# Performance work log

Hardware: AMD Instinct MI355X
Metric: run time of the kernel (lower is better)

## Reference

```python
import jax, jax.numpy as jnp
import numpy as np

D_MODEL = 512
N_HEADS = 4  # d_model >= 8 -> 4 heads
HEAD_DIM = D_MODEL // N_HEADS
D_FF = 4 * D_MODEL


def setup_inputs() -> dict:
    key = jax.random.key(0)
    ks = jax.random.split(key, 8)
    B, T = 4, 2048
    s = 0.02
    return {
        "x": jax.random.normal(ks[0], (B, T, D_MODEL), dtype=jnp.float32),
        "ln1_g": jnp.ones((D_MODEL,), jnp.float32),
        "ln1_b": jnp.zeros((D_MODEL,), jnp.float32),
        "w_qkv": jax.random.normal(ks[1], (D_MODEL, 3 * D_MODEL), jnp.float32) * s,
        "w_proj": jax.random.normal(ks[2], (D_MODEL, D_MODEL), jnp.float32) * s,
        "ln2_g": jnp.ones((D_MODEL,), jnp.float32),
        "ln2_b": jnp.zeros((D_MODEL,), jnp.float32),
        "w_ff1": jax.random.normal(ks[3], (D_MODEL, D_FF), jnp.float32) * s,
        "w_ff2": jax.random.normal(ks[4], (D_FF, D_MODEL), jnp.float32) * s,
    }


def _layernorm(x, g, b, eps=1e-5):
    mu = jnp.mean(x, axis=-1, keepdims=True)
    var = jnp.var(x, axis=-1, keepdims=True)
    return (x - mu) * jax.lax.rsqrt(var + eps) * g + b


def _attention(x, w_qkv, w_proj):
    B, T, C = x.shape
    qkv = x @ w_qkv  # [B,T,3C]
    q, k, v = jnp.split(qkv, 3, axis=-1)
    # [B,H,T,Dh]
    q = q.reshape(B, T, N_HEADS, HEAD_DIM).transpose(0, 2, 1, 3)
    k = k.reshape(B, T, N_HEADS, HEAD_DIM).transpose(0, 2, 1, 3)
    v = v.reshape(B, T, N_HEADS, HEAD_DIM).transpose(0, 2, 1, 3)
    scale = 1.0 / jnp.sqrt(jnp.asarray(HEAD_DIM, x.dtype))
    scores = jnp.einsum("bhqd,bhkd->bhqk", q, k) * scale
    causal = jnp.tril(jnp.ones((T, T), bool))
    scores = jnp.where(causal, scores, -jnp.inf)
    attn = jax.nn.softmax(scores, axis=-1)
    out = jnp.einsum("bhqk,bhkd->bhqd", attn, v)
    out = out.transpose(0, 2, 1, 3).reshape(B, T, C)
    return out @ w_proj


def reference(x, ln1_g, ln1_b, w_qkv, w_proj, ln2_g, ln2_b, w_ff1, w_ff2):
    x = x + _attention(_layernorm(x, ln1_g, ln1_b), w_qkv, w_proj)
    h = _layernorm(x, ln2_g, ln2_b)
    h = jax.nn.gelu(h @ w_ff1, approximate=False) @ w_ff2
    return x + h
```

## Files before the change

kernel.cpp:

```cpp
#include <hip/hip_runtime.h>
#include <cstdint>

typedef unsigned short u16;
typedef __attribute__((ext_vector_type(8))) short short8;
typedef __attribute__((ext_vector_type(4))) float floatx4;

#define BT    8192
#define TSEQ  2048
#define NBAT  4
#define CMOD  512
#define NH    4
#define HD    128
#define DFF   2048
#define CQKV  1536

__device__ __forceinline__ u16 f2bf(float f) {
  union { float f; uint32_t u; } v; v.f = f;
  uint32_t r = v.u + 0x7FFFu + ((v.u >> 16) & 1u);
  return (u16)(r >> 16);
}

__device__ __forceinline__ float exp2a(float x) {
  float r; asm("v_exp_f32 %0, %1" : "=v"(r) : "v"(x)); return r;
}
__device__ __forceinline__ float rcpa(float x) {
  float r; asm("v_rcp_f32 %0, %1" : "=v"(r) : "v"(x)); return r;
}

typedef __attribute__((address_space(1))) const unsigned int ga_u32;
typedef __attribute__((address_space(3))) unsigned int ls_u32;
__device__ __forceinline__ void glds16(const u16* g, u16* l) {
  __builtin_amdgcn_global_load_lds((ga_u32*)g, (ls_u32*)l, 16, 0, 0);
}

__global__ __launch_bounds__(256) void transpose_cast(const float* __restrict__ W,
                                                      u16* __restrict__ Wt, int K, int N) {
  __shared__ float tile[32][33];
  int n0 = blockIdx.x * 32, k0 = blockIdx.y * 32;
  int tx = threadIdx.x & 31, ty = threadIdx.x >> 5;
  #pragma unroll
  for (int r = 0; r < 32; r += 8)
    tile[r + ty][tx] = W[(size_t)(k0 + r + ty) * N + n0 + tx];
  __syncthreads();
  #pragma unroll
  for (int r = 0; r < 32; r += 8)
    Wt[(size_t)(n0 + r + ty) * K + k0 + tx] = f2bf(tile[tx][r + ty]);
}

__global__ __launch_bounds__(256) void ln_kernel(const float* __restrict__ x,
                                                 const float* __restrict__ g,
                                                 const float* __restrict__ b,
                                                 u16* __restrict__ out) {
  int row = blockIdx.x * 4 + (threadIdx.x >> 6);
  int lane = threadIdx.x & 63;
  const float4* xr = (const float4*)(x + (size_t)row * CMOD);
  float4 a = xr[lane], c = xr[lane + 64];
  float s = a.x + a.y + a.z + a.w + c.x + c.y + c.z + c.w;
  float q = a.x*a.x + a.y*a.y + a.z*a.z + a.w*a.w
          + c.x*c.x + c.y*c.y + c.z*c.z + c.w*c.w;
  #pragma unroll
  for (int o = 32; o; o >>= 1) { s += __shfl_xor(s, o); q += __shfl_xor(q, o); }
  float mu = s * (1.0f / CMOD);
  float rstd = rsqrtf(q * (1.0f / CMOD) - mu * mu + 1e-5f);
  const float4* gr = (const float4*)g;
  const float4* br = (const float4*)b;
  float4 g0 = gr[lane], g1 = gr[lane + 64], b0 = br[lane], b1 = br[lane + 64];
  u16* orow = out + (size_t)row * CMOD;
  int i0 = lane * 4, i1 = (lane + 64) * 4;
  orow[i0 + 0] = f2bf((a.x - mu) * rstd * g0.x + b0.x);
  orow[i0 + 1] = f2bf((a.y - mu) * rstd * g0.y + b0.y);
  orow[i0 + 2] = f2bf((a.z - mu) * rstd * g0.z + b0.z);
  orow[i0 + 3] = f2bf((a.w - mu) * rstd * g0.w + b0.w);
  orow[i1 + 0] = f2bf((c.x - mu) * rstd * g1.x + b1.x);
  orow[i1 + 1] = f2bf((c.y - mu) * rstd * g1.y + b1.y);
  orow[i1 + 2] = f2bf((c.z - mu) * rstd * g1.z + b1.z);
  orow[i1 + 3] = f2bf((c.w - mu) * rstd * g1.w + b1.w);
}

template <int EPI>
__global__ __launch_bounds__(256) void gemm_kernel(
    const u16* __restrict__ A, const u16* __restrict__ Bt, int K,
    const float* __restrict__ resid, float* __restrict__ outf,
    u16* __restrict__ ob0, u16* __restrict__ ob1, u16* __restrict__ ob2) {
  constexpr int LDT = 40;
  __shared__ __align__(16) u16 As[128 * LDT];
  __shared__ __align__(16) u16 Bs[128 * LDT];
  int tid = threadIdx.x;
  int lane = tid & 63, wave = tid >> 6;
  int lane16 = lane & 15, quad = lane >> 4;
  int m0 = blockIdx.y * 128, n0 = blockIdx.x * 128;
  int wm = (wave >> 1) * 64, wn = (wave & 1) * 64;
  int srow = tid >> 2, skc = (tid & 3) * 8;

  floatx4 acc[4][4];
  #pragma unroll
  for (int i = 0; i < 4; i++)
    #pragma unroll
    for (int j = 0; j < 4; j++) acc[i][j] = (floatx4)(0.0f);

  const u16* Arow0 = A + (size_t)(m0 + srow) * K + skc;
  const u16* Arow1 = A + (size_t)(m0 + srow + 64) * K + skc;
  const u16* Brow0 = Bt + (size_t)(n0 + srow) * K + skc;
  const u16* Brow1 = Bt + (size_t)(n0 + srow + 64) * K + skc;

  for (int k0 = 0; k0 < K; k0 += 32) {
    __syncthreads();
    *(short8*)&As[srow * LDT + skc]        = *(const short8*)(Arow0 + k0);
    *(short8*)&As[(srow + 64) * LDT + skc] = *(const short8*)(Arow1 + k0);
    *(short8*)&Bs[srow * LDT + skc]        = *(const short8*)(Brow0 + k0);
    *(short8*)&Bs[(srow + 64) * LDT + skc] = *(const short8*)(Brow1 + k0);
    __syncthreads();
    short8 af[4], bf[4];
    #pragma unroll
    for (int i = 0; i < 4; i++)
      af[i] = *(const short8*)&As[(wm + i * 16 + lane16) * LDT + quad * 8];
    #pragma unroll
    for (int j = 0; j < 4; j++)
      bf[j] = *(const short8*)&Bs[(wn + j * 16 + lane16) * LDT + quad * 8];
    #pragma unroll
    for (int i = 0; i < 4; i++)
      #pragma unroll
      for (int j = 0; j < 4; j++)
        acc[i][j] = __builtin_amdgcn_mfma_f32_16x16x32_bf16(af[i], bf[j], acc[i][j], 0, 0, 0);
  }

  #pragma unroll
  for (int i = 0; i < 4; i++) {
    #pragma unroll
    for (int j = 0; j < 4; j++) {
      #pragma unroll
      for (int r = 0; r < 4; r++) {
        int m = m0 + wm + i * 16 + quad * 4 + r;
        int n = n0 + wn + j * 16 + lane16;
        float v = acc[i][j][r];
        if (EPI == 0) {
          int bb = m >> 11, t = m & 2047;
          int nn = n & 511, which = n >> 9;
          int h = nn >> 7, d = nn & 127;
          size_t bh = (size_t)(bb * NH + h);
          if (which == 0)      ob0[bh * TSEQ * HD + (size_t)t * HD + d] = f2bf(v * 0.12751743f);
          else if (which == 1) ob1[bh * TSEQ * HD + (size_t)t * HD + d] = f2bf(v);
          else                 ob2[bh * HD * TSEQ + (size_t)d * TSEQ + t] = f2bf(v);
        } else if (EPI == 1) {
          size_t idx = (size_t)m * CMOD + n;
          outf[idx] = v + resid[idx];
        } else if (EPI == 2) {
          float ge = 0.5f * v * (1.0f + erff(v * 0.70710678118654752f));
          ob0[(size_t)m * DFF + n] = f2bf(ge);
        } else {
          size_t idx = (size_t)m * CMOD + n;
          outf[idx] = v + resid[idx];
        }
      }
    }
  }
}

__global__ __launch_bounds__(256) void attn_kernel(const u16* __restrict__ qb,
                                                   const u16* __restrict__ kb,
                                                   const u16* __restrict__ vtb,
                                                   u16* __restrict__ ob) {
  __shared__ __align__(16) u16 Ks[32 * 128];
  __shared__ __align__(16) u16 Vs[128 * 32];
  __shared__ __align__(16) uint32_t Ps[4 * 16 * 20];
  int tid = threadIdx.x, wave = tid >> 6, lane = tid & 63;
  int lane16 = lane & 15, quad = lane >> 4;
  int bh = blockIdx.x;
  int qt = 31 - (int)blockIdx.y;
  int q0w = qt * 64 + wave * 16;
  const u16* Q  = qb  + (size_t)bh * TSEQ * HD;
  const u16* Kg = kb  + (size_t)bh * TSEQ * HD;
  const u16* Vg = vtb + (size_t)bh * HD * TSEQ;

  short8 aq[4];
  {
    int qrow = q0w + lane16;
    #pragma unroll
    for (int cc = 0; cc < 4; cc++)
      aq[cc] = *(const short8*)&Q[(size_t)qrow * HD + cc * 32 + quad * 8];
  }

  const u16* kgp[2]; const u16* vgp[2]; u16* klp[2]; u16* vlp[2];
  #pragma unroll
  for (int i = 0; i < 2; i++) {
    int s = wave * 128 + i * 64 + lane;
    int r = s >> 4, cp = s & 15, c = cp ^ (r & 7);
    kgp[i] = Kg + (size_t)r * HD + c * 8;
    klp[i] = Ks + (size_t)(wave * 128 + i * 64) * 8;
    int d = s >> 2, cv = (s & 3) ^ ((d >> 1) & 3);
    vgp[i] = Vg + (size_t)d * TSEQ + cv * 8;
    vlp[i] = Vs + (size_t)(wave * 128 + i * 64) * 8;
  }

  int ktw = (q0w >> 5) + 1;
  int ktblk = ((qt * 64 + 48) >> 5) + 1;

  floatx4 o[8];
  #pragma unroll
  for (int j = 0; j < 8; j++) o[j] = (floatx4)(0.0f);
  floatx4 ol = (floatx4)(0.0f);

  short8 ones;
  #pragma unroll
  for (int e = 0; e < 8; e++) ones[e] = (short)0x3F80;

  uint32_t* Pw = &Ps[wave * 320];
  int swl = lane16 & 7;
  int cvr = quad ^ ((lane16 >> 1) & 3);

  for (int kt = 0; kt < ktblk; kt++) {
    __syncthreads();
    glds16(kgp[0] + (size_t)kt * 32 * HD, klp[0]);
    glds16(kgp[1] + (size_t)kt * 32 * HD, klp[1]);
    glds16(vgp[0] + kt * 32, vlp[0]);
    glds16(vgp[1] + kt * 32, vlp[1]);
    __syncthreads();
    if (kt >= ktw) continue;

    floatx4 st0 = (floatx4)(0.0f), st1 = (floatx4)(0.0f);
    #pragma unroll
    for (int cc = 0; cc < 4; cc++) {
      short8 kf0 = *(const short8*)&Ks[(lane16 * 16 + ((cc * 4 + quad) ^ swl)) * 8];
      short8 kf1 = *(const short8*)&Ks[((16 + lane16) * 16 + ((cc * 4 + quad) ^ swl)) * 8];
      st0 = __builtin_amdgcn_mfma_f32_16x16x32_bf16(aq[cc], kf0, st0, 0, 0, 0);
      st1 = __builtin_amdgcn_mfma_f32_16x16x32_bf16(aq[cc], kf1, st1, 0, 0, 0);
    }
    short8 vf[8];
    #pragma unroll
    for (int j = 0; j < 8; j++)
      vf[j] = *(const short8*)&Vs[((j * 16 + lane16) * 4 + cvr) * 8];

    int kg0 = kt * 32 + lane16;
    #pragma unroll
    for (int r = 0; r < 4; r++) {
      int qr = q0w + quad * 4 + r;
      float p0 = exp2a(st0[r]);
      float p1 = exp2a(st1[r]);
      if (kg0 > qr) p0 = 0.0f;
      if (kg0 + 16 > qr) p1 = 0.0f;
      Pw[(quad * 4 + r) * 20 + lane16] =
          __builtin_amdgcn_perm(__float_as_uint(p1), __float_as_uint(p0), 0x07060302u);
    }
    asm volatile("s_waitcnt lgkmcnt(0)" ::: "memory");

    union { uint32_t u[4]; short8 s; } pf;
    {
      const uint32_t* prow = &Pw[lane16 * 20 + (quad & 1) * 8];
      uint32_t d0 = prow[0], d1 = prow[1], d2 = prow[2], d3 = prow[3];
      uint32_t d4 = prow[4], d5 = prow[5], d6 = prow[6], d7 = prow[7];
      uint32_t sel = (quad >> 1) ? 0x07060302u : 0x05040100u;
      pf.u[0] = __builtin_amdgcn_perm(d1, d0, sel);
      pf.u[1] = __builtin_amdgcn_perm(d3, d2, sel);
      pf.u[2] = __builtin_amdgcn_perm(d5, d4, sel);
      pf.u[3] = __builtin_amdgcn_perm(d7, d6, sel);
    }
    #pragma unroll
    for (int j = 0; j < 8; j++)
      o[j] = __builtin_amdgcn_mfma_f32_16x16x32_bf16(pf.s, vf[j], o[j], 0, 0, 0);
    ol = __builtin_amdgcn_mfma_f32_16x16x32_bf16(pf.s, ones, ol, 0, 0, 0);
  }

  int bb = bh >> 2, h = bh & 3;
  #pragma unroll
  for (int r = 0; r < 4; r++) {
    int t = q0w + quad * 4 + r;
    float inv = rcpa(ol[r]);
    #pragma unroll
    for (int j = 0; j < 8; j++)
      ob[((size_t)(bb * TSEQ + t)) * CMOD + h * HD + j * 16 + lane16] = f2bf(o[j][r] * inv);
  }
}

extern "C" void kernel_launch(void* const* d_in, const int* in_sizes, int n_in,
                              void* d_out, int out_size, void* d_ws, size_t ws_size,
                              hipStream_t stream) {
  const float* x     = (const float*)d_in[0];
  const float* ln1g  = (const float*)d_in[1];
  const float* ln1b  = (const float*)d_in[2];
  const float* wqkv  = (const float*)d_in[3];
  const float* wproj = (const float*)d_in[4];
  const float* ln2g  = (const float*)d_in[5];
  const float* ln2b  = (const float*)d_in[6];
  const float* wff1  = (const float*)d_in[7];
  const float* wff2  = (const float*)d_in[8];
  float* out = (float*)d_out;
  char* ws = (char*)d_ws;

  u16* wt_qkv  = (u16*)(ws);
  u16* wt_proj = (u16*)(ws + 1572864);
  u16* wt_ff1  = (u16*)(ws + 2097152);
  u16* wt_ff2  = (u16*)(ws + 4194304);
  u16* ln_buf  = (u16*)(ws + 6291456);
  u16* q_buf   = (u16*)(ws + 14680064);
  u16* k_buf   = (u16*)(ws + 23068672);
  u16* vt_buf  = (u16*)(ws + 31457280);
  u16* attn    = (u16*)(ws + 39845888);
  float* x2    = (float*)(ws + 48234496);
  u16* h1      = (u16*)(ws + 65011712);

  dim3 blk(256);
  transpose_cast<<<dim3(CQKV / 32, CMOD / 32), blk, 0, stream>>>(wqkv, wt_qkv, CMOD, CQKV);
  transpose_cast<<<dim3(CMOD / 32, CMOD / 32), blk, 0, stream>>>(wproj, wt_proj, CMOD, CMOD);
  transpose_cast<<<dim3(DFF / 32, CMOD / 32), blk, 0, stream>>>(wff1, wt_ff1, CMOD, DFF);
  transpose_cast<<<dim3(CMOD / 32, DFF / 32), blk, 0, stream>>>(wff2, wt_ff2, DFF, CMOD);

  ln_kernel<<<dim3(BT / 4), blk, 0, stream>>>(x, ln1g, ln1b, ln_buf);

  gemm_kernel<0><<<dim3(CQKV / 128, BT / 128), blk, 0, stream>>>(
      ln_buf, wt_qkv, CMOD, nullptr, nullptr, q_buf, k_buf, vt_buf);

  attn_kernel<<<dim3(NBAT * NH, TSEQ / 64), blk, 0, stream>>>(q_buf, k_buf, vt_buf, attn);

  gemm_kernel<1><<<dim3(CMOD / 128, BT / 128), blk, 0, stream>>>(
      attn, wt_proj, CMOD, x, x2, nullptr, nullptr, nullptr);

  ln_kernel<<<dim3(BT / 4), blk, 0, stream>>>(x2, ln2g, ln2b, ln_buf);

  gemm_kernel<2><<<dim3(DFF / 128, BT / 128), blk, 0, stream>>>(
      ln_buf, wt_ff1, CMOD, nullptr, nullptr, h1, nullptr, nullptr);

  gemm_kernel<3><<<dim3(CMOD / 128, BT / 128), blk, 0, stream>>>(
      h1, wt_ff2, DFF, x2, out, nullptr, nullptr, nullptr);
}
```

Baseline: 295.4 us.

## Double-buffer GEMM and attention tiles with async LDS loads, narrow N tiles

The GEMM kernel now copies its tiles straight from global memory into LDS with glds16 into two alternating buffers. The next K tile is prefetched while the current one is multiplied, so there is one barrier per iteration instead of two. The attention kernel gets the same double-buffered K/V prefetch. The N-tile width becomes a template parameter, and the two GEMMs with a 512-wide output use 64-wide tiles so they launch more blocks. The LDS row padding is removed to match the direct-load layout, which may cause bank conflicts on fragment reads, and the doubled LDS use may lower occupancy.

```diff
diff --git a/kernel.cpp b/kernel.cpp
--- a/kernel.cpp
+++ b/kernel.cpp
@@ -77,57 +77,78 @@
   orow[i1 + 3] = f2bf((c.w - mu) * rstd * g1.w + b1.w);
 }
 
-template <int EPI>
+template <int EPI, int TN>
 __global__ __launch_bounds__(256) void gemm_kernel(
     const u16* __restrict__ A, const u16* __restrict__ Bt, int K,
     const float* __restrict__ resid, float* __restrict__ outf,
     u16* __restrict__ ob0, u16* __restrict__ ob1, u16* __restrict__ ob2) {
-  constexpr int LDT = 40;
-  __shared__ __align__(16) u16 As[128 * LDT];
-  __shared__ __align__(16) u16 Bs[128 * LDT];
+  constexpr int WNF = TN / 32;
+  constexpr int NKB = TN / 64;
+  __shared__ __align__(16) u16 As[2][128 * 32];
+  __shared__ __align__(16) u16 Bs[2][TN * 32];
   int tid = threadIdx.x;
   int lane = tid & 63, wave = tid >> 6;
   int lane16 = lane & 15, quad = lane >> 4;
-  int m0 = blockIdx.y * 128, n0 = blockIdx.x * 128;
-  int wm = (wave >> 1) * 64, wn = (wave & 1) * 64;
-  int srow = tid >> 2, skc = (tid & 3) * 8;
-
-  floatx4 acc[4][4];
+  int m0 = blockIdx.y * 128, n0 = blockIdx.x * TN;
+  int wm = (wave >> 1) * 64, wn = (wave & 1) * (TN / 2);
+
+  floatx4 acc[4][WNF];
   #pragma unroll
   for (int i = 0; i < 4; i++)
     #pragma unroll
-    for (int j = 0; j < 4; j++) acc[i][j] = (floatx4)(0.0f);
-
-  const u16* Arow0 = A + (size_t)(m0 + srow) * K + skc;
-  const u16* Arow1 = A + (size_t)(m0 + srow + 64) * K + skc;
-  const u16* Brow0 = Bt + (size_t)(n0 + srow) * K + skc;
-  const u16* Brow1 = Bt + (size_t)(n0 + srow + 64) * K + skc;
-
-  for (int k0 = 0; k0 < K; k0 += 32) {
+    for (int j = 0; j < WNF; j++) acc[i][j] = (floatx4)(0.0f);
+
+  const u16* agp[2]; u16* alp[2][2];
+  const u16* bgp[NKB]; u16* blp[NKB][2];
+  #pragma unroll
+  for (int i = 0; i < 2; i++) {
+    int s = i * 256 + tid;
+    agp[i] = A + (size_t)(m0 + (s >> 2)) * K + (s & 3) * 8;
+    alp[i][0] = &As[0][(i * 256 + wave * 64) * 8];
+    alp[i][1] = &As[1][(i * 256 + wave * 64) * 8];
+  }
+  #pragma unroll
+  for (int i = 0; i < NKB; i++) {
+    int s = i * 256 + tid;
+    bgp[i] = Bt + (size_t)(n0 + (s >> 2)) * K + (s & 3) * 8;
+    blp[i][0] = &Bs[0][(i * 256 + wave * 64) * 8];
+    blp[i][1] = &Bs[1][(i * 256 + wave * 64) * 8];
+  }
+
+  int nk = K >> 5;
+  #pragma unroll
+  for (int i = 0; i < 2; i++) glds16(agp[i], alp[i][0]);
+  #pragma unroll
+  for (int i = 0; i < NKB; i++) glds16(bgp[i], blp[i][0]);
+
+  for (int kt = 0; kt < nk; kt++) {
     __syncthreads();
-    *(short8*)&As[srow * LDT + skc]        = *(const short8*)(Arow0 + k0);
-    *(short8*)&As[(srow + 64) * LDT + skc] = *(const short8*)(Arow1 + k0);
-    *(short8*)&Bs[srow * LDT + skc]        = *(const short8*)(Brow0 + k0);
-    *(short8*)&Bs[(srow + 64) * LDT + skc] = *(const short8*)(Brow1 + k0);
-    __syncthreads();
-    short8 af[4], bf[4];
+    int buf = kt & 1;
+    if (kt + 1 < nk) {
+      int k1 = (kt + 1) * 32;
+      #pragma unroll
+      for (int i = 0; i < 2; i++) glds16(agp[i] + k1, alp[i][buf ^ 1]);
+      #pragma unroll
+      for (int i = 0; i < NKB; i++) glds16(bgp[i] + k1, blp[i][buf ^ 1]);
+    }
+    short8 af[4], bf[WNF];
     #pragma unroll
     for (int i = 0; i < 4; i++)
-      af[i] = *(const short8*)&As[(wm + i * 16 + lane16) * LDT + quad * 8];
-    #pragma unroll
-    for (int j = 0; j < 4; j++)
-      bf[j] = *(const short8*)&Bs[(wn + j * 16 + lane16) * LDT + quad * 8];
+      af[i] = *(const short8*)&As[buf][(wm + i * 16 + lane16) * 32 + quad * 8];
+    #pragma unroll
+    for (int j = 0; j < WNF; j++)
+      bf[j] = *(const short8*)&Bs[buf][(wn + j * 16 + lane16) * 32 + quad * 8];
     #pragma unroll
     for (int i = 0; i < 4; i++)
       #pragma unroll
-      for (int j = 0; j < 4; j++)
+      for (int j = 0; j < WNF; j++)
         acc[i][j] = __builtin_amdgcn_mfma_f32_16x16x32_bf16(af[i], bf[j], acc[i][j], 0, 0, 0);
   }
 
   #pragma unroll
   for (int i = 0; i < 4; i++) {
     #pragma unroll
-    for (int j = 0; j < 4; j++) {
+    for (int j = 0; j < WNF; j++) {
       #pragma unroll
       for (int r = 0; r < 4; r++) {
         int m = m0 + wm + i * 16 + quad * 4 + r;
@@ -160,8 +181,8 @@
                                                    const u16* __restrict__ kb,
                                                    const u16* __restrict__ vtb,
                                                    u16* __restrict__ ob) {
-  __shared__ __align__(16) u16 Ks[32 * 128];
-  __shared__ __align__(16) u16 Vs[128 * 32];
+  __shared__ __align__(16) u16 Ks[2][32 * 128];
+  __shared__ __align__(16) u16 Vs[2][128 * 32];
   __shared__ __align__(16) uint32_t Ps[4 * 16 * 20];
   int tid = threadIdx.x, wave = tid >> 6, lane = tid & 63;
   int lane16 = lane & 15, quad = lane >> 4;
@@ -180,20 +201,24 @@
       aq[cc] = *(const short8*)&Q[(size_t)qrow * HD + cc * 32 + quad * 8];
   }
 
-  const u16* kgp[2]; const u16* vgp[2]; u16* klp[2]; u16* vlp[2];
+  const u16* kgp[2]; const u16* vgp[2];
+  u16* klp[2][2]; u16* vlp[2][2];
   #pragma unroll
   for (int i = 0; i < 2; i++) {
     int s = wave * 128 + i * 64 + lane;
     int r = s >> 4, cp = s & 15, c = cp ^ (r & 7);
     kgp[i] = Kg + (size_t)r * HD + c * 8;
-    klp[i] = Ks + (size_t)(wave * 128 + i * 64) * 8;
     int d = s >> 2, cv = (s & 3) ^ ((d >> 1) & 3);
     vgp[i] = Vg + (size_t)d * TSEQ + cv * 8;
-    vlp[i] = Vs + (size_t)(wave * 128 + i * 64) * 8;
+    #pragma unroll
+    for (int bfr = 0; bfr < 2; bfr++) {
+      klp[i][bfr] = &Ks[bfr][(wave * 128 + i * 64) * 8];
+      vlp[i][bfr] = &Vs[bfr][(wave * 128 + i * 64) * 8];
+    }
   }
 
   int ktw = (q0w >> 5) + 1;
-  int ktblk = ((qt * 64 + 48) >> 5) + 1;
+  int ktblk = qt * 2 + 2;
 
   floatx4 o[8];
   #pragma unroll
@@ -208,27 +233,34 @@
   int swl = lane16 & 7;
   int cvr = quad ^ ((lane16 >> 1) & 3);
 
+  #pragma unroll
+  for (int i = 0; i < 2; i++) { glds16(kgp[i], klp[i][0]); glds16(vgp[i], vlp[i][0]); }
+
   for (int kt = 0; kt < ktblk; kt++) {
     __syncthreads();
-    glds16(kgp[0] + (size_t)kt * 32 * HD, klp[0]);
-    glds16(kgp[1] + (size_t)kt * 32 * HD, klp[1]);
-    glds16(vgp[0] + kt * 32, vlp[0]);
-    glds16(vgp[1] + kt * 32, vlp[1]);
-    __syncthreads();
+    int buf = kt & 1;
+    if (kt + 1 < ktblk) {
+      int ko = (kt + 1) * 32;
+      #pragma unroll
+      for (int i = 0; i < 2; i++) {
+        glds16(kgp[i] + (size_t)ko * HD, klp[i][buf ^ 1]);
+        glds16(vgp[i] + ko, vlp[i][buf ^ 1]);
+      }
+    }
     if (kt >= ktw) continue;
 
     floatx4 st0 = (floatx4)(0.0f), st1 = (floatx4)(0.0f);
     #pragma unroll
     for (int cc = 0; cc < 4; cc++) {
-      short8 kf0 = *(const short8*)&Ks[(lane16 * 16 + ((cc * 4 + quad) ^ swl)) * 8];
-      short8 kf1 = *(const short8*)&Ks[((16 + lane16) * 16 + ((cc * 4 + quad) ^ swl)) * 8];
+      short8 kf0 = *(const short8*)&Ks[buf][(lane16 * 16 + ((cc * 4 + quad) ^ swl)) * 8];
+      short8 kf1 = *(const short8*)&Ks[buf][((16 + lane16) * 16 + ((cc * 4 + quad) ^ swl)) * 8];
       st0 = __builtin_amdgcn_mfma_f32_16x16x32_bf16(aq[cc], kf0, st0, 0, 0, 0);
       st1 = __builtin_amdgcn_mfma_f32_16x16x32_bf16(aq[cc], kf1, st1, 0, 0, 0);
     }
     short8 vf[8];
     #pragma unroll
     for (int j = 0; j < 8; j++)
-      vf[j] = *(const short8*)&Vs[((j * 16 + lane16) * 4 + cvr) * 8];
+      vf[j] = *(const short8*)&Vs[buf][((j * 16 + lane16) * 4 + cvr) * 8];
 
     int kg0 = kt * 32 + lane16;
     #pragma unroll
@@ -306,19 +338,19 @@
 
   ln_kernel<<<dim3(BT / 4), blk, 0, stream>>>(x, ln1g, ln1b, ln_buf);
 
-  gemm_kernel<0><<<dim3(CQKV / 128, BT / 128), blk, 0, stream>>>(
+  gemm_kernel<0, 128><<<dim3(CQKV / 128, BT / 128), blk, 0, stream>>>(
       ln_buf, wt_qkv, CMOD, nullptr, nullptr, q_buf, k_buf, vt_buf);
 
   attn_kernel<<<dim3(NBAT * NH, TSEQ / 64), blk, 0, stream>>>(q_buf, k_buf, vt_buf, attn);
 
-  gemm_kernel<1><<<dim3(CMOD / 128, BT / 128), blk, 0, stream>>>(
+  gemm_kernel<1, 64><<<dim3(CMOD / 64, BT / 128), blk, 0, stream>>>(
       attn, wt_proj, CMOD, x, x2, nullptr, nullptr, nullptr);
 
   ln_kernel<<<dim3(BT / 4), blk, 0, stream>>>(x2, ln2g, ln2b, ln_buf);
 
-  gemm_kernel<2><<<dim3(DFF / 128, BT / 128), blk, 0, stream>>>(
+  gemm_kernel<2, 128><<<dim3(DFF / 128, BT / 128), blk, 0, stream>>>(
       ln_buf, wt_ff1, CMOD, nullptr, nullptr, h1, nullptr, nullptr);
 
-  gemm_kernel<3><<<dim3(CMOD / 128, BT / 128), blk, 0, stream>>>(
+  gemm_kernel<3, 64><<<dim3(CMOD / 64, BT / 128), blk, 0, stream>>>(
       h1, wt_ff2, DFF, x2, out, nullptr, nullptr, nullptr);
 }
```

New measurement: 285.3 us. 1.04x faster.
